# Performance work log

Hardware: AMD Instinct MI355X
Metric: run time of the kernel (lower is better)

Reference implementation:

```python
import jax, jax.numpy as jnp
import numpy as np

N_NODES = 100000
N_REL = 4
N_EDGES = 500000
D_IN = 128
D_OUT = 128


def setup_inputs() -> dict:
    key = jax.random.key(0)
    k1, k2, k3, k4 = jax.random.split(key, 4)
    x = jax.random.normal(k1, (N_NODES, D_IN), dtype=jnp.float32)
    W = jax.random.normal(k2, (N_REL, D_IN, D_OUT), dtype=jnp.float32) * (1.0 / np.sqrt(D_IN))
    b = jnp.zeros((N_REL, D_OUT), dtype=jnp.float32)
    src_idx = jax.random.randint(k3, (N_REL, N_EDGES), 0, N_NODES)
    dst_idx = jax.random.randint(k4, (N_REL, N_EDGES), 0, N_NODES)
    return {"x": x, "W": W, "b": b, "src_idx": src_idx, "dst_idx": dst_idx}


def reference(x, W, b, src_idx, dst_idx):
    # RGCN layer: per-relation GraphConv(norm='right') -> sum over relations -> ReLU.
    # GraphConv(norm='right'): aggregate src features into dst, divide by dst in-degree,
    # apply weight (in_feats == out_feats so DGL aggregates first, then matmuls), add bias.
    n = x.shape[0]

    def per_relation(src, dst, Wr, br):
        # gather src features [E, D_IN] and scatter-sum into dst rows [N, D_IN]
        agg = jax.ops.segment_sum(x[src], dst, num_segments=n)
        deg = jax.ops.segment_sum(jnp.ones(dst.shape, dtype=x.dtype), dst, num_segments=n)
        agg = agg / jnp.maximum(deg, 1.0)[:, None]  # norm='right'
        return agg @ Wr + br  # [N, D_OUT]

    outs = jax.vmap(per_relation)(src_idx, dst_idx, W, b)  # [R, N, D_OUT]
    h = outs.sum(axis=0)  # HeteroGraphConv aggregate='sum'
    return jax.nn.relu(h)
```

## Files before the change

### kernel.cpp

```cpp
#include <hip/hip_runtime.h>

#define D 128
#define NREL 4
#define BINSHIFT 8
#define NBK 256
#define BCAP 1664
#define BPAD 32

typedef __attribute__((ext_vector_type(8))) short short8;
typedef __attribute__((ext_vector_type(4))) float f32x4;

static __device__ inline unsigned short f2bf(float f) {
    unsigned int u = __float_as_uint(f);
    u += 0x7fffu + ((u >> 16) & 1u);
    return (unsigned short)(u >> 16);
}

__global__ __launch_bounds__(256) void part1prep_kernel(
    const float* __restrict__ x,
    const float* __restrict__ W,
    const float* __restrict__ bias,
    const int* __restrict__ src, const int* __restrict__ dst,
    int* __restrict__ binCnt, unsigned int* __restrict__ part,
    unsigned short* __restrict__ xB,
    unsigned short* __restrict__ Wsw,
    float* __restrict__ bsum,
    int E, int N, int nbins, int total)
{
    const int t     = threadIdx.x;
    const int gtid  = blockIdx.x * 256 + t;
    const int gsize = gridDim.x * 256;
    const int E2 = 2 * E, E3 = 3 * E;

    const int nq = total >> 2;
    for (int i = gtid; i < nq; i += gsize) {
        const int e = i * 4;
        const int4 s4 = ((const int4*)src)[i];
        const int4 d4 = ((const int4*)dst)[i];
        #pragma unroll
        for (int k = 0; k < 4; ++k) {
            const int ek = e + k;
            const int sk = (k == 0) ? s4.x : (k == 1) ? s4.y : (k == 2) ? s4.z : s4.w;
            const int dk = (k == 0) ? d4.x : (k == 1) ? d4.y : (k == 2) ? d4.z : d4.w;
            const int r  = (ek >= E) + (ek >= E2) + (ek >= E3);
            const int g  = (dk << 2) | r;
            const unsigned entry = (unsigned)sk | ((unsigned)(g & (NBK - 1)) << 17);
            const int bin = g >> BINSHIFT;
            const int pos = atomicAdd(&binCnt[bin * BPAD], 1);
            if (pos < BCAP)
                part[(size_t)bin * BCAP + pos] = entry;
        }
    }
    for (int e = (nq << 2) + gtid; e < total; e += gsize) {
        const int r  = (e >= E) + (e >= E2) + (e >= E3);
        const int g  = (dst[e] << 2) | r;
        const unsigned entry = (unsigned)src[e] | ((unsigned)(g & (NBK - 1)) << 17);
        const int bin = g >> BINSHIFT;
        const int pos = atomicAdd(&binCnt[bin * BPAD], 1);
        if (pos < BCAP)
            part[(size_t)bin * BCAP + pos] = entry;
    }

    if (gtid < D)
        bsum[gtid] = bias[gtid] + bias[D + gtid] + bias[2 * D + gtid] + bias[3 * D + gtid];

    for (int gid = gtid; gid < 8192; gid += gsize) {
        const int l   = gid & 63;
        const int ct  = (gid >> 6) & 7;
        const int kb  = gid >> 9;
        const int rel = kb >> 2;
        const int kbase = (kb & 3) * 32 + (l >> 4) * 8;
        const int nn = ct * 16 + (l & 15);
        ushort4 v0, v1;
        const float* wp = W + (size_t)rel * D * D + (size_t)kbase * D + nn;
        v0.x = f2bf(wp[0 * D]); v0.y = f2bf(wp[1 * D]);
        v0.z = f2bf(wp[2 * D]); v0.w = f2bf(wp[3 * D]);
        v1.x = f2bf(wp[4 * D]); v1.y = f2bf(wp[5 * D]);
        v1.z = f2bf(wp[6 * D]); v1.w = f2bf(wp[7 * D]);
        ushort4* op = (ushort4*)(Wsw + (size_t)gid * 8);
        op[0] = v0;
        op[1] = v1;
    }

    const int n4 = N * D / 4;
    for (int i = gtid; i < n4; i += gsize) {
        const float4 v = ((const float4*)x)[i];
        ushort4 o;
        o.x = f2bf(v.x); o.y = f2bf(v.y); o.z = f2bf(v.z); o.w = f2bf(v.w);
        ((ushort4*)xB)[i] = o;
    }
}

__global__ __launch_bounds__(256, 8) void agg_gemm_kernel(
    const unsigned int* __restrict__ part,
    const int* __restrict__ binCnt,
    const unsigned short* __restrict__ xB,
    const unsigned short* __restrict__ Wsw,
    const float* __restrict__ bsum,
    float* __restrict__ out,
    int N)
{
    __shared__ int sh_s[BCAP];
    __shared__ int hist[NBK];
    __shared__ int scanbuf[NBK];
    __shared__ int offl[NBK + 1];
    __shared__ __align__(16) unsigned short agg[32 * 128];
    unsigned int* raw = (unsigned int*)agg;

    const int t    = threadIdx.x;
    const int b    = blockIdx.x;
    const size_t base = (size_t)b * BCAP;
    const int cnt  = min(binCnt[b * BPAD], BCAP);
    const int dst0 = b * 64;

    hist[t] = 0;
    __syncthreads();
    for (int i = t; i < cnt; i += 256) {
        const unsigned v = part[base + i];
        raw[i] = v;
        atomicAdd(&hist[v >> 17], 1);
    }
    __syncthreads();

    const int myc = hist[t];
    scanbuf[t] = myc;
    __syncthreads();
    for (int off = 1; off < 256; off <<= 1) {
        int v = (t >= off) ? scanbuf[t - off] : 0;
        __syncthreads();
        scanbuf[t] += v;
        __syncthreads();
    }
    offl[t] = scanbuf[t] - myc;
    if (t == 255) offl[256] = scanbuf[255];
    hist[t] = scanbuf[t] - myc;
    __syncthreads();

    for (int i = t; i < cnt; i += 256) {
        const unsigned v = raw[i];
        const int pos = atomicAdd(&hist[v >> 17], 1);
        sh_s[pos] = (int)(v & 0x1FFFF);
    }
    __syncthreads();

    const int c    = t & 15;
    const int team = t >> 4;

    const int wv   = t >> 6;
    const int l    = t & 63;
    const int lrow = l & 15;
    const int quad = l >> 4;
    const int ct0  = wv * 2;

    #define ACCUM(v)                                        \
        accL[0] += __uint_as_float((v).x << 16);            \
        accH[0] += __uint_as_float((v).x & 0xffff0000u);    \
        accL[1] += __uint_as_float((v).y << 16);            \
        accH[1] += __uint_as_float((v).y & 0xffff0000u);    \
        accL[2] += __uint_as_float((v).z << 16);            \
        accH[2] += __uint_as_float((v).z & 0xffff0000u);    \
        accL[3] += __uint_as_float((v).w << 16);            \
        accH[3] += __uint_as_float((v).w & 0xffff0000u);

    #pragma unroll 1
    for (int h = 0; h < 2; ++h) {
        f32x4 acc[2][2] = {};

        #pragma unroll 1
        for (int q = 0; q < NREL; ++q) {
            if (h | q) __syncthreads();

            for (int ld = team; ld < 32; ld += 16) {
                const int bkt = (h * 32 + ld) * 4 + q;
                const int beg = offl[bkt];
                const int end = offl[bkt + 1];
                const float inv = 1.0f / fmaxf((float)(end - beg), 1.0f);

                float accL[4] = {0.f, 0.f, 0.f, 0.f};
                float accH[4] = {0.f, 0.f, 0.f, 0.f};

                int j = beg;
                for (; j + 3 < end; j += 4) {
                    const int s0 = sh_s[j];
                    const int s1 = sh_s[j + 1];
                    const int s2 = sh_s[j + 2];
                    const int s3 = sh_s[j + 3];
                    const uint4 v0 = *(const uint4*)(xB + (size_t)s0 * D + c * 8);
                    const uint4 v1 = *(const uint4*)(xB + (size_t)s1 * D + c * 8);
                    const uint4 v2 = *(const uint4*)(xB + (size_t)s2 * D + c * 8);
                    const uint4 v3 = *(const uint4*)(xB + (size_t)s3 * D + c * 8);
                    ACCUM(v0) ACCUM(v1) ACCUM(v2) ACCUM(v3)
                }
                for (; j < end; ++j) {
                    const uint4 v0 = *(const uint4*)(xB + (size_t)sh_s[j] * D + c * 8);
                    ACCUM(v0)
                }

                uint4 o;
                o.x = ((unsigned)f2bf(accH[0] * inv) << 16) | f2bf(accL[0] * inv);
                o.y = ((unsigned)f2bf(accH[1] * inv) << 16) | f2bf(accL[1] * inv);
                o.z = ((unsigned)f2bf(accH[2] * inv) << 16) | f2bf(accL[2] * inv);
                o.w = ((unsigned)f2bf(accH[3] * inv) << 16) | f2bf(accL[3] * inv);
                const int byte = (c * 16) ^ ((ld & 7) << 4);
                *(uint4*)((char*)agg + ld * 256 + byte) = o;
            }
            __syncthreads();

            #pragma unroll
            for (int kbl = 0; kbl < 4; ++kbl) {
                short8 a[2];
                #pragma unroll
                for (int rt = 0; rt < 2; ++rt) {
                    const int row  = rt * 16 + lrow;
                    const int byte = (kbl * 64 + quad * 16) ^ ((row & 7) << 4);
                    a[rt] = *(const short8*)((const char*)agg + row * 256 + byte);
                }
                const int kb = q * 4 + kbl;
                const unsigned short* wp = Wsw + ((size_t)(kb * 8 + ct0) * 64 + l) * 8;
                const short8 b0 = *(const short8*)wp;
                const short8 b1 = *(const short8*)(wp + 64 * 8);
                acc[0][0] = __builtin_amdgcn_mfma_f32_16x16x32_bf16(a[0], b0, acc[0][0], 0, 0, 0);
                acc[1][0] = __builtin_amdgcn_mfma_f32_16x16x32_bf16(a[1], b0, acc[1][0], 0, 0, 0);
                acc[0][1] = __builtin_amdgcn_mfma_f32_16x16x32_bf16(a[0], b1, acc[0][1], 0, 0, 0);
                acc[1][1] = __builtin_amdgcn_mfma_f32_16x16x32_bf16(a[1], b1, acc[1][1], 0, 0, 0);
            }
        }

        #pragma unroll
        for (int ci = 0; ci < 2; ++ci) {
            const int col = (ct0 + ci) * 16 + lrow;
            const float bv = bsum[col];
            #pragma unroll
            for (int rt = 0; rt < 2; ++rt) {
                #pragma unroll
                for (int e = 0; e < 4; ++e) {
                    const int row = dst0 + h * 32 + rt * 16 + quad * 4 + e;
                    if (row < N)
                        out[(size_t)row * D + col] = fmaxf(acc[rt][ci][e] + bv, 0.f);
                }
            }
        }
    }
    #undef ACCUM
}

static inline size_t align_up(size_t v, size_t a) { return (v + a - 1) & ~(a - 1); }

extern "C" void kernel_launch(void* const* d_in, const int* in_sizes, int n_in,
                              void* d_out, int out_size, void* d_ws, size_t ws_size,
                              hipStream_t stream)
{
    const float* x    = (const float*)d_in[0];
    const float* W    = (const float*)d_in[1];
    const float* bias = (const float*)d_in[2];
    const int* src    = (const int*)d_in[3];
    const int* dst    = (const int*)d_in[4];
    float* out        = (float*)d_out;

    const int N = in_sizes[0] / D;
    const int E = in_sizes[3] / NREL;
    const int nG = NREL * N;
    const int totalE = NREL * E;
    const int nbins  = (nG + NBK - 1) >> BINSHIFT;

    char* w = (char*)d_ws;
    int* binCnt = (int*)w;            w += align_up((size_t)nbins * BPAD * 4, 256);
    unsigned int* part = (unsigned int*)w;     w += align_up((size_t)nbins * BCAP * 4, 256);
    unsigned short* Wsw = (unsigned short*)w;  w += align_up((size_t)512 * D * 2, 256);
    float* bsum = (float*)w;          w += align_up((size_t)D * 4, 256);
    unsigned short* xB = (unsigned short*)w;

    const int p1_blocks = 2048;

    hipMemsetAsync(binCnt, 0, (size_t)nbins * BPAD * sizeof(int), stream);
    part1prep_kernel<<<p1_blocks, 256, 0, stream>>>(
        x, W, bias, src, dst, binCnt, part, xB, Wsw, bsum, E, N, nbins, totalE);
    agg_gemm_kernel<<<nbins, 256, 0, stream>>>(part, binCnt, xB, Wsw, bsum, out, N);
}
```

Measured before the change: 292.2 us.

## Replace global per-edge atomics with block-local histogram and bulk bin reservation

The edge partitioning step now uses only the first 128 blocks. Each block takes a contiguous chunk of edges, builds a bin histogram in LDS, reserves space per bin with one global atomic, then scatters entries using LDS atomics for positions. This replaces one global atomic per edge (2M total) with one per bin per block, at the cost of reading dst twice and using less of the grid for this phase. The int4 vectorized loads are dropped.

```diff
diff --git a/kernel.cpp b/kernel.cpp
--- a/kernel.cpp
+++ b/kernel.cpp
@@ -6,6 +6,8 @@
 #define NBK 256
 #define BCAP 1664
 #define BPAD 32
+#define NSCAT 128
+#define NBINS_MAX 1600
 
 typedef __attribute__((ext_vector_type(8))) short short8;
 typedef __attribute__((ext_vector_type(4))) float f32x4;
@@ -27,38 +29,43 @@
     float* __restrict__ bsum,
     int E, int N, int nbins, int total)
 {
+    __shared__ int hist[NBINS_MAX];
+
     const int t     = threadIdx.x;
     const int gtid  = blockIdx.x * 256 + t;
     const int gsize = gridDim.x * 256;
     const int E2 = 2 * E, E3 = 3 * E;
 
-    const int nq = total >> 2;
-    for (int i = gtid; i < nq; i += gsize) {
-        const int e = i * 4;
-        const int4 s4 = ((const int4*)src)[i];
-        const int4 d4 = ((const int4*)dst)[i];
-        #pragma unroll
-        for (int k = 0; k < 4; ++k) {
-            const int ek = e + k;
-            const int sk = (k == 0) ? s4.x : (k == 1) ? s4.y : (k == 2) ? s4.z : s4.w;
-            const int dk = (k == 0) ? d4.x : (k == 1) ? d4.y : (k == 2) ? d4.z : d4.w;
-            const int r  = (ek >= E) + (ek >= E2) + (ek >= E3);
-            const int g  = (dk << 2) | r;
-            const unsigned entry = (unsigned)sk | ((unsigned)(g & (NBK - 1)) << 17);
+    if (blockIdx.x < NSCAT) {
+        const int chunk = (total + NSCAT - 1) / NSCAT;
+        const int e0 = blockIdx.x * chunk;
+        const int n  = min(chunk, total - e0);
+
+        for (int i = t; i < nbins; i += 256) hist[i] = 0;
+        __syncthreads();
+
+        for (int i = t; i < n; i += 256) {
+            const int e = e0 + i;
+            const int g = (dst[e] << 2) | ((e >= E) + (e >= E2) + (e >= E3));
+            atomicAdd(&hist[g >> BINSHIFT], 1);
+        }
+        __syncthreads();
+
+        for (int b = t; b < nbins; b += 256) {
+            const int h = hist[b];
+            hist[b] = h ? b * BCAP + atomicAdd(&binCnt[b * BPAD], h) : 0;
+        }
+        __syncthreads();
+
+        for (int i = t; i < n; i += 256) {
+            const int e = e0 + i;
+            const int g = (dst[e] << 2) | ((e >= E) + (e >= E2) + (e >= E3));
             const int bin = g >> BINSHIFT;
-            const int pos = atomicAdd(&binCnt[bin * BPAD], 1);
-            if (pos < BCAP)
-                part[(size_t)bin * BCAP + pos] = entry;
-        }
-    }
-    for (int e = (nq << 2) + gtid; e < total; e += gsize) {
-        const int r  = (e >= E) + (e >= E2) + (e >= E3);
-        const int g  = (dst[e] << 2) | r;
-        const unsigned entry = (unsigned)src[e] | ((unsigned)(g & (NBK - 1)) << 17);
-        const int bin = g >> BINSHIFT;
-        const int pos = atomicAdd(&binCnt[bin * BPAD], 1);
-        if (pos < BCAP)
-            part[(size_t)bin * BCAP + pos] = entry;
+            const unsigned entry = (unsigned)src[e] | ((unsigned)(g & (NBK - 1)) << 17);
+            const int pos = atomicAdd(&hist[bin], 1);
+            if (pos < (bin + 1) * BCAP)
+                part[pos] = entry;
+        }
     }
 
     if (gtid < D)
```

New measurement: 283.6 us. 1.03x faster.
